# Optimization experiments

Measured on AMD Instinct MI355X. Metric: run time of the kernel, lower is better.

## Reference

```python
import jax, jax.numpy as jnp
import numpy as np

BLOCK_SIZE = 16
# Signed NVFP4 (e2m1) value table; code = sign_bit<<3 | magnitude_index
FP4_VALUES = jnp.array(
    [0.0, 0.5, 1.0, 1.5, 2.0, 3.0, 4.0, 6.0,
     -0.0, -0.5, -1.0, -1.5, -2.0, -3.0, -4.0, -6.0],
    dtype=jnp.float32)


def setup_inputs() -> dict:
    key = jax.random.key(0)
    k1, k2, k3 = jax.random.split(key, 3)
    O, I = 4096, 4096
    x = jax.random.normal(k1, (2, 1024, I), dtype=jnp.float32)
    # per-block scales (positive), one per 16-element block along in_features
    weight_scales = jax.random.uniform(k2, (O, I // BLOCK_SIZE), dtype=jnp.float32,
                                       minval=0.01, maxval=1.0)
    weight_q = jax.random.randint(k3, (O, I), 0, 16, dtype=jnp.int32)
    return {"x": x, "weight_scales": weight_scales, "weight_q": weight_q}


def dequantize_nvfp4_sim(weight_q, weight_scales, block_size=BLOCK_SIZE):
    O, I = weight_q.shape
    vals = FP4_VALUES[weight_q]                              # [O, I] fp32 e2m1 values
    w = vals.reshape(O, I // block_size, block_size) * weight_scales[:, :, None]
    return w.reshape(O, I)


def reference(x, weight_scales, weight_q):
    # Dequantize NVFP4 -> BF16, then BF16 GEMM (F.linear), cast back to input dtype.
    w = dequantize_nvfp4_sim(weight_q, weight_scales).astype(jnp.bfloat16)  # [O, I]
    x_bf16 = x.astype(jnp.bfloat16)
    out = jnp.einsum('bsi,oi->bso', x_bf16, w)               # [B, S, O] bf16
    return out.astype(x.dtype)
```

## Files before the change

### kernel.cpp

```cpp
#include <hip/hip_runtime.h>

typedef __bf16  bf16x8 __attribute__((ext_vector_type(8)));
typedef float   f32x4  __attribute__((ext_vector_type(4)));
typedef short   short8 __attribute__((ext_vector_type(8)));

static __device__ __forceinline__ unsigned short f2bf(float f) {
  union { float f; unsigned int u; } v; v.f = f;
  unsigned int u = v.u;
  u += 0x7fffu + ((u >> 16) & 1u);
  return (unsigned short)(u >> 16);
}

static __device__ __forceinline__ float fp4_decode(int qc) {
  int e = (qc >> 1) & 3;
  float m = (float)(qc & 1);
  float mag = (e == 0) ? (0.5f * m)
                       : ((2.0f + m) * 0.5f * (float)(1 << (e - 1)));
  return (qc & 8) ? -mag : mag;
}

__global__ __launch_bounds__(256) void w4a16_prep(
    const int* __restrict__ wq, const float* __restrict__ wsc,
    short* __restrict__ wout, int nblkW,
    const float* __restrict__ x, short* __restrict__ xb, int n8) {
  const int nbW = nblkW >> 8;
  if ((int)blockIdx.x < nbW) {
    int idx = blockIdx.x * 256 + threadIdx.x;
    if (idx >= nblkW) return;
    float s = wsc[idx];
    const int4* qp = (const int4*)wq + (size_t)idx * 4;
    int4 q0 = qp[0], q1 = qp[1], q2 = qp[2], q3 = qp[3];
    short8 r0, r1;
    r0[0] = (short)f2bf(fp4_decode(q0.x) * s);
    r0[1] = (short)f2bf(fp4_decode(q0.y) * s);
    r0[2] = (short)f2bf(fp4_decode(q0.z) * s);
    r0[3] = (short)f2bf(fp4_decode(q0.w) * s);
    r0[4] = (short)f2bf(fp4_decode(q1.x) * s);
    r0[5] = (short)f2bf(fp4_decode(q1.y) * s);
    r0[6] = (short)f2bf(fp4_decode(q1.z) * s);
    r0[7] = (short)f2bf(fp4_decode(q1.w) * s);
    r1[0] = (short)f2bf(fp4_decode(q2.x) * s);
    r1[1] = (short)f2bf(fp4_decode(q2.y) * s);
    r1[2] = (short)f2bf(fp4_decode(q2.z) * s);
    r1[3] = (short)f2bf(fp4_decode(q2.w) * s);
    r1[4] = (short)f2bf(fp4_decode(q3.x) * s);
    r1[5] = (short)f2bf(fp4_decode(q3.y) * s);
    r1[6] = (short)f2bf(fp4_decode(q3.z) * s);
    r1[7] = (short)f2bf(fp4_decode(q3.w) * s);
    short8* op = (short8*)wout + (size_t)idx * 2;
    op[0] = r0;
    op[1] = r1;
  } else {
    int idx = (blockIdx.x - nbW) * 256 + threadIdx.x;
    if (idx >= n8) return;
    const float4* xp = (const float4*)x + (size_t)idx * 2;
    float4 a = xp[0], b = xp[1];
    short8 r;
    r[0] = (short)f2bf(a.x); r[1] = (short)f2bf(a.y);
    r[2] = (short)f2bf(a.z); r[3] = (short)f2bf(a.w);
    r[4] = (short)f2bf(b.x); r[5] = (short)f2bf(b.y);
    r[6] = (short)f2bf(b.z); r[7] = (short)f2bf(b.w);
    ((short8*)xb)[idx] = r;
  }
}

#define BM 128
#define BN 256
#define BK 64
#define NBUF 3
#define ASZ (BM * BK)
#define BSZ (BN * BK)

__global__ __launch_bounds__(512, 1) void w4a16_gemm_ra(
    const short* __restrict__ A, const short* __restrict__ B,
    float* __restrict__ C, int M, int N, int K) {
  __shared__ __attribute__((aligned(16))) short As[NBUF * ASZ];
  __shared__ __attribute__((aligned(16))) short Bs[NBUF * BSZ];

  const int tid  = threadIdx.x;
  const int lane = tid & 63;
  const int wid  = tid >> 6;
  const int wr   = wid >> 2;
  const int wc   = wid & 3;

  const int bm = blockIdx.y * BM;
  const int bn = blockIdx.x * BN;

  f32x4 acc[4][4] = {};

  const int fr    = lane & 15;
  const int klane = lane >> 4;
  const int xv    = fr & 7;

  const size_t rowbytes = (size_t)K * 2;

  size_t aoff[2];  int aldso[2];
#pragma unroll
  for (int r = 0; r < 2; ++r) {
    int u = r * 512 + tid;
    int row = u >> 3, c = u & 7;
    int csrc = c ^ (row & 7);
    aoff[r]  = (size_t)(bm + row) * rowbytes + (size_t)csrc * 16;
    aldso[r] = u * 16;
  }
  size_t boff[4];  int bldso[4];
#pragma unroll
  for (int r = 0; r < 4; ++r) {
    int u = r * 512 + tid;
    int row = u >> 3, c = u & 7;
    int csrc = c ^ (row & 7);
    boff[r]  = (size_t)(bn + row) * rowbytes + (size_t)csrc * 16;
    bldso[r] = u * 16;
  }

  const char* Ag = (const char*)A;
  const char* Bg = (const char*)B;

#define STAGE_A(bufbase, koff2, r)                                              \
  __builtin_amdgcn_global_load_lds(                                             \
      (const __attribute__((address_space(1))) unsigned int*)(Ag + aoff[r] + (koff2)), \
      (__attribute__((address_space(3))) unsigned int*)((char*)(bufbase) + aldso[r]),  \
      16, 0, 0)
#define STAGE_B(bufbase, koff2, r)                                              \
  __builtin_amdgcn_global_load_lds(                                             \
      (const __attribute__((address_space(1))) unsigned int*)(Bg + boff[r] + (koff2)), \
      (__attribute__((address_space(3))) unsigned int*)((char*)(bufbase) + bldso[r]),  \
      16, 0, 0)

  auto readA = [&](const short* Ab, int mi, int kk) -> bf16x8 {
    int row = wr * 64 + mi * 16 + fr;
    int c = kk * 4 + klane;
    return *(const bf16x8*)((const char*)Ab + (size_t)row * 128 + ((c ^ xv) << 4));
  };
  auto readB = [&](const short* Bb, int ni, int kk) -> bf16x8 {
    int row = wc * 64 + ni * 16 + fr;
    int c = kk * 4 + klane;
    return *(const bf16x8*)((const char*)Bb + (size_t)row * 128 + ((c ^ xv) << 4));
  };

  const int NT = K / BK;

  bf16x8 afA[4][2], bfA[4][2], afB[4][2], bfB[4][2];

  {
    char* A0 = (char*)As; char* B0 = (char*)Bs;
    char* A1 = (char*)(As + ASZ); char* B1 = (char*)(Bs + BSZ);
    STAGE_A(A0, 0, 0); STAGE_A(A0, 0, 1);
    STAGE_B(B0, 0, 0); STAGE_B(B0, 0, 1); STAGE_B(B0, 0, 2); STAGE_B(B0, 0, 3);
    size_t k2 = (size_t)BK * 2;
    STAGE_A(A1, k2, 0); STAGE_A(A1, k2, 1);
    STAGE_B(B1, k2, 0); STAGE_B(B1, k2, 1); STAGE_B(B1, k2, 2); STAGE_B(B1, k2, 3);
  }
  __builtin_amdgcn_sched_barrier(0);
  asm volatile("s_waitcnt vmcnt(6)");
  __builtin_amdgcn_s_barrier();
  __builtin_amdgcn_sched_barrier(0);
#pragma unroll
  for (int mi = 0; mi < 4; ++mi)
#pragma unroll
    for (int kk = 0; kk < 2; ++kk)
      afA[mi][kk] = readA(As, mi, kk);
#pragma unroll
  for (int ni = 0; ni < 4; ++ni)
#pragma unroll
    for (int kk = 0; kk < 2; ++kk)
      bfA[ni][kk] = readB(Bs, ni, kk);

  int nr = 1, ns = 2;

#define TILE_BODY(t_, AFU, BFU, AFL, BFL)                                       \
  do {                                                                          \
    if ((t_) + 2 < NT) {                                                        \
      char* An = (char*)(As + ns * ASZ);                                        \
      char* Bn = (char*)(Bs + ns * BSZ);                                        \
      const size_t ko_ = (size_t)((t_) + 2) * (BK * 2);                         \
      STAGE_A(An, ko_, 0); STAGE_A(An, ko_, 1);                                 \
      STAGE_B(Bn, ko_, 0); STAGE_B(Bn, ko_, 1);                                 \
      STAGE_B(Bn, ko_, 2); STAGE_B(Bn, ko_, 3);                                 \
    }                                                                           \
    __builtin_amdgcn_s_setprio(1);                                              \
    _Pragma("unroll") for (int mi = 0; mi < 2; ++mi)                            \
      _Pragma("unroll") for (int ni = 0; ni < 4; ++ni)                          \
        _Pragma("unroll") for (int kk = 0; kk < 2; ++kk)                        \
          acc[mi][ni] = __builtin_amdgcn_mfma_f32_16x16x32_bf16(                \
              AFU[mi][kk], BFU[ni][kk], acc[mi][ni], 0, 0, 0);                  \
    __builtin_amdgcn_s_setprio(0);                                              \
    __builtin_amdgcn_sched_barrier(0);                                          \
    if ((t_) + 1 < NT) {                                                        \
      if ((t_) + 2 < NT) asm volatile("s_waitcnt vmcnt(6)");                    \
      else               asm volatile("s_waitcnt vmcnt(0)");                    \
      __builtin_amdgcn_s_barrier();                       \
      __builtin_amdgcn_sched_barrier(0);                                        \
      const short* Ar = As + nr * ASZ;                                          \
      const short* Br = Bs + nr * BSZ;                                          \
      _Pragma("unroll") for (int mi = 0; mi < 4; ++mi)                          \
        _Pragma("unroll") for (int kk = 0; kk < 2; ++kk)                        \
          AFL[mi][kk] = readA(Ar, mi, kk);                                      \
      _Pragma("unroll") for (int ni = 0; ni < 4; ++ni)                          \
        _Pragma("unroll") for (int kk = 0; kk < 2; ++kk)                        \
          BFL[ni][kk] = readB(Br, ni, kk);                                      \
      __builtin_amdgcn_sched_barrier(0);                                        \
    }                                                                           \
    __builtin_amdgcn_s_setprio(1);                                              \
    _Pragma("unroll") for (int mi = 2; mi < 4; ++mi)                            \
      _Pragma("unroll") for (int ni = 0; ni < 4; ++ni)                          \
        _Pragma("unroll") for (int kk = 0; kk < 2; ++kk)                        \
          acc[mi][ni] = __builtin_amdgcn_mfma_f32_16x16x32_bf16(                \
              AFU[mi][kk], BFU[ni][kk], acc[mi][ni], 0, 0, 0);                  \
    __builtin_amdgcn_s_setprio(0);                                              \
    nr = ns; ns = (ns == NBUF - 1) ? 0 : ns + 1;                                \
  } while (0)

  for (int t = 0; t < NT; t += 2) {
    TILE_BODY(t,     afA, bfA, afB, bfB);
    TILE_BODY(t + 1, afB, bfB, afA, bfA);
  }

  const int cn = lane & 15;
  const int rb = (lane >> 4) * 4;
#pragma unroll
  for (int ai = 0; ai < 4; ++ai)
#pragma unroll
    for (int bj = 0; bj < 4; ++bj) {
      int m0 = bm + wr * 64 + ai * 16 + rb;
      int n0 = bn + wc * 64 + bj * 16 + cn;
#pragma unroll
      for (int r = 0; r < 4; ++r)
        C[(size_t)(m0 + r) * N + n0] = acc[ai][bj][r];
    }
}

extern "C" void kernel_launch(void* const* d_in, const int* in_sizes, int n_in,
                              void* d_out, int out_size, void* d_ws, size_t ws_size,
                              hipStream_t stream) {
  const float* x   = (const float*)d_in[0];
  const float* wsc = (const float*)d_in[1];
  const int*   wq  = (const int*)d_in[2];
  float* out = (float*)d_out;

  const int K = 4096;
  const int N = in_sizes[2] / K;
  const int M = in_sizes[0] / K;

  short* Wb = (short*)d_ws;
  short* Xb = Wb + (size_t)N * K;

  int nblkW = (N * K) / 16;
  int n8    = (M * K) / 8;
  int gridP = (nblkW >> 8) + ((n8 + 255) >> 8);
  w4a16_prep<<<gridP, 256, 0, stream>>>(wq, wsc, Wb, nblkW, x, Xb, n8);

  dim3 grid(N / BN, M / BM);
  w4a16_gemm_ra<<<grid, 512, 0, stream>>>(Xb, Wb, out, M, N, K);
}
```

Before: 90.07 us.

## Restructure GEMM main loop into one-ahead prefetch with interleaved LDS reads

Replaces the two-tile-ahead prefetch loop with a one-ahead schedule. Each iteration waits for all outstanding global loads, issues the next tile's loads, and interleaves LDS fragment reads for the current tile with MFMAs on the previous tile's fragments, draining with a final MFMA block. Launch bounds change to request two workgroups per CU, which caps registers per thread. LDS still allocates three buffers (96KB), so two blocks may not fit per CU. The full vmcnt(0) wait each iteration also gives up load latency hiding.

```diff
diff --git a/kernel.cpp b/kernel.cpp
--- a/kernel.cpp
+++ b/kernel.cpp
@@ -71,7 +71,7 @@
 #define ASZ (BM * BK)
 #define BSZ (BN * BK)
 
-__global__ __launch_bounds__(512, 1) void w4a16_gemm_ra(
+__global__ __launch_bounds__(512, 2) void w4a16_gemm_dp(
     const short* __restrict__ A, const short* __restrict__ B,
     float* __restrict__ C, int M, int N, int K) {
   __shared__ __attribute__((aligned(16))) short As[NBUF * ASZ];
@@ -142,79 +142,80 @@
 
   bf16x8 afA[4][2], bfA[4][2], afB[4][2], bfB[4][2];
 
+  int cur = 0, nxt = 1;
+
   {
     char* A0 = (char*)As; char* B0 = (char*)Bs;
-    char* A1 = (char*)(As + ASZ); char* B1 = (char*)(Bs + BSZ);
     STAGE_A(A0, 0, 0); STAGE_A(A0, 0, 1);
     STAGE_B(B0, 0, 0); STAGE_B(B0, 0, 1); STAGE_B(B0, 0, 2); STAGE_B(B0, 0, 3);
-    size_t k2 = (size_t)BK * 2;
-    STAGE_A(A1, k2, 0); STAGE_A(A1, k2, 1);
-    STAGE_B(B1, k2, 0); STAGE_B(B1, k2, 1); STAGE_B(B1, k2, 2); STAGE_B(B1, k2, 3);
-  }
-  __builtin_amdgcn_sched_barrier(0);
-  asm volatile("s_waitcnt vmcnt(6)");
-  __builtin_amdgcn_s_barrier();
-  __builtin_amdgcn_sched_barrier(0);
-#pragma unroll
-  for (int mi = 0; mi < 4; ++mi)
-#pragma unroll
-    for (int kk = 0; kk < 2; ++kk)
-      afA[mi][kk] = readA(As, mi, kk);
-#pragma unroll
-  for (int ni = 0; ni < 4; ++ni)
-#pragma unroll
-    for (int kk = 0; kk < 2; ++kk)
-      bfA[ni][kk] = readB(Bs, ni, kk);
-
-  int nr = 1, ns = 2;
-
-#define TILE_BODY(t_, AFU, BFU, AFL, BFL)                                       \
+  }
+
+#define ITER(i_, RDA, RDB, MFA, MFB, DO_MFMA)                                   \
   do {                                                                          \
-    if ((t_) + 2 < NT) {                                                        \
-      char* An = (char*)(As + ns * ASZ);                                        \
-      char* Bn = (char*)(Bs + ns * BSZ);                                        \
-      const size_t ko_ = (size_t)((t_) + 2) * (BK * 2);                         \
+    asm volatile("s_waitcnt vmcnt(0)");        \
+    __builtin_amdgcn_s_barrier();           \
+    if ((i_) + 1 < NT) {                                                        \
+      char* An = (char*)(As + nxt * ASZ);                                       \
+      char* Bn = (char*)(Bs + nxt * BSZ);                                       \
+      const size_t ko_ = (size_t)((i_) + 1) * (BK * 2);                         \
       STAGE_A(An, ko_, 0); STAGE_A(An, ko_, 1);                                 \
       STAGE_B(Bn, ko_, 0); STAGE_B(Bn, ko_, 1);                                 \
       STAGE_B(Bn, ko_, 2); STAGE_B(Bn, ko_, 3);                                 \
     }                                                                           \
-    __builtin_amdgcn_s_setprio(1);                                              \
-    _Pragma("unroll") for (int mi = 0; mi < 2; ++mi)                            \
+    __builtin_amdgcn_sched_barrier(0);                                          \
+    {                                                                           \
+      const short* Ac = As + cur * ASZ;                                         \
+      _Pragma("unroll") for (int mi = 0; mi < 4; ++mi)                          \
+        _Pragma("unroll") for (int kk = 0; kk < 2; ++kk)                        \
+          RDA[mi][kk] = readA(Ac, mi, kk);                                      \
+    }                                                                           \
+    __builtin_amdgcn_sched_barrier(0);                                          \
+    if (DO_MFMA) {                                                              \
+      __builtin_amdgcn_s_setprio(1);                                            \
+      _Pragma("unroll") for (int mi = 0; mi < 2; ++mi)                          \
+        _Pragma("unroll") for (int ni = 0; ni < 4; ++ni)                        \
+          _Pragma("unroll") for (int kk = 0; kk < 2; ++kk)                      \
+            acc[mi][ni] = __builtin_amdgcn_mfma_f32_16x16x32_bf16(              \
+                MFA[mi][kk], MFB[ni][kk], acc[mi][ni], 0, 0, 0);                \
+      __builtin_amdgcn_s_setprio(0);                                            \
+    }                                                                           \
+    __builtin_amdgcn_sched_barrier(0);                                          \
+    {                                                                           \
+      const short* Bc = Bs + cur * BSZ;                                         \
       _Pragma("unroll") for (int ni = 0; ni < 4; ++ni)                          \
         _Pragma("unroll") for (int kk = 0; kk < 2; ++kk)                        \
-          acc[mi][ni] = __builtin_amdgcn_mfma_f32_16x16x32_bf16(                \
-              AFU[mi][kk], BFU[ni][kk], acc[mi][ni], 0, 0, 0);                  \
-    __builtin_amdgcn_s_setprio(0);                                              \
-    __builtin_amdgcn_sched_barrier(0);                                          \
-    if ((t_) + 1 < NT) {                                                        \
-      if ((t_) + 2 < NT) asm volatile("s_waitcnt vmcnt(6)");                    \
-      else               asm volatile("s_waitcnt vmcnt(0)");                    \
-      __builtin_amdgcn_s_barrier();                       \
-      __builtin_amdgcn_sched_barrier(0);                                        \
-      const short* Ar = As + nr * ASZ;                                          \
-      const short* Br = Bs + nr * BSZ;                                          \
-      _Pragma("unroll") for (int mi = 0; mi < 4; ++mi)                          \
-        _Pragma("unroll") for (int kk = 0; kk < 2; ++kk)                        \
-          AFL[mi][kk] = readA(Ar, mi, kk);                                      \
-      _Pragma("unroll") for (int ni = 0; ni < 4; ++ni)                          \
-        _Pragma("unroll") for (int kk = 0; kk < 2; ++kk)                        \
-          BFL[ni][kk] = readB(Br, ni, kk);                                      \
-      __builtin_amdgcn_sched_barrier(0);                                        \
-    }                                                                           \
-    __builtin_amdgcn_s_setprio(1);                                              \
-    _Pragma("unroll") for (int mi = 2; mi < 4; ++mi)                            \
-      _Pragma("unroll") for (int ni = 0; ni < 4; ++ni)                          \
-        _Pragma("unroll") for (int kk = 0; kk < 2; ++kk)                        \
-          acc[mi][ni] = __builtin_amdgcn_mfma_f32_16x16x32_bf16(                \
-              AFU[mi][kk], BFU[ni][kk], acc[mi][ni], 0, 0, 0);                  \
-    __builtin_amdgcn_s_setprio(0);                                              \
-    nr = ns; ns = (ns == NBUF - 1) ? 0 : ns + 1;                                \
+          RDB[ni][kk] = readB(Bc, ni, kk);                                      \
+    }                                                                           \
+    __builtin_amdgcn_sched_barrier(0);                                          \
+    if (DO_MFMA) {                                                              \
+      __builtin_amdgcn_s_setprio(1);                                            \
+      _Pragma("unroll") for (int mi = 2; mi < 4; ++mi)                          \
+        _Pragma("unroll") for (int ni = 0; ni < 4; ++ni)                        \
+          _Pragma("unroll") for (int kk = 0; kk < 2; ++kk)                      \
+            acc[mi][ni] = __builtin_amdgcn_mfma_f32_16x16x32_bf16(              \
+                MFA[mi][kk], MFB[ni][kk], acc[mi][ni], 0, 0, 0);                \
+      __builtin_amdgcn_s_setprio(0);                                            \
+    }                                                                           \
+    cur = (cur == NBUF - 1) ? 0 : cur + 1;                                      \
+    nxt = (nxt == NBUF - 1) ? 0 : nxt + 1;                                      \
   } while (0)
 
-  for (int t = 0; t < NT; t += 2) {
-    TILE_BODY(t,     afA, bfA, afB, bfB);
-    TILE_BODY(t + 1, afB, bfB, afA, bfA);
-  }
+  ITER(0, afA, bfA, afB, bfB, 0);
+  ITER(1, afB, bfB, afA, bfA, 1);
+  for (int t = 2; t < NT; t += 2) {
+    ITER(t,     afA, bfA, afB, bfB, 1);
+    ITER(t + 1, afB, bfB, afA, bfA, 1);
+  }
+  __builtin_amdgcn_s_setprio(1);
+#pragma unroll
+  for (int mi = 0; mi < 4; ++mi)
+#pragma unroll
+    for (int ni = 0; ni < 4; ++ni)
+#pragma unroll
+      for (int kk = 0; kk < 2; ++kk)
+        acc[mi][ni] = __builtin_amdgcn_mfma_f32_16x16x32_bf16(
+            afB[mi][kk], bfB[ni][kk], acc[mi][ni], 0, 0, 0);
+  __builtin_amdgcn_s_setprio(0);
 
   const int cn = lane & 15;
   const int rb = (lane >> 4) * 4;
@@ -251,5 +252,5 @@
   w4a16_prep<<<gridP, 256, 0, stream>>>(wq, wsc, Wb, nblkW, x, Xb, n8);
 
   dim3 grid(N / BN, M / BM);
-  w4a16_gemm_ra<<<grid, 512, 0, stream>>>(Xb, Wb, out, M, N, K);
-}
+  w4a16_gemm_dp<<<grid, 512, 0, stream>>>(Xb, Wb, out, M, N, K);
+}
```

Result: slower. 109.6 us (+21.7%).
